# Optimization experiments

Measured on AMD Instinct MI355X. Metric: run time of the kernel, lower is better.

## Reference

```python
import jax, jax.numpy as jnp
import numpy as np

C_M, C_Z, C_H = 256, 128, 32
EPS = 1e-3      # outer-product-mean normalization eps
LN_EPS = 1e-5   # LayerNorm eps (torch default)


def setup_inputs() -> dict:
    key = jax.random.key(0)
    ks = jax.random.split(key, 8)
    B, S, R = 1, 128, 256
    m = jax.random.normal(ks[0], (B, S, R, C_M), dtype=jnp.float32)
    mask = jnp.ones((B, S, R), dtype=jnp.float32)
    ln_g = jnp.ones((C_M,), dtype=jnp.float32)
    ln_b = jnp.zeros((C_M,), dtype=jnp.float32)
    w1 = jax.random.normal(ks[1], (C_M, C_H), dtype=jnp.float32) * (1.0 / np.sqrt(C_M))
    b1 = jnp.zeros((C_H,), dtype=jnp.float32)
    w2 = jax.random.normal(ks[2], (C_M, C_H), dtype=jnp.float32) * (1.0 / np.sqrt(C_M))
    b2 = jnp.zeros((C_H,), dtype=jnp.float32)
    # linear_out uses init='final' (zeros) in training; use small random for a nontrivial baseline
    w_out = jax.random.normal(ks[3], (C_H * C_H, C_Z), dtype=jnp.float32) * 0.02
    b_out = jnp.zeros((C_Z,), dtype=jnp.float32)
    return {"m": m, "mask": mask, "ln_g": ln_g, "ln_b": ln_b,
            "w1": w1, "b1": b1, "w2": w2, "b2": b2,
            "w_out": w_out, "b_out": b_out}


def reference(m, mask, ln_g, ln_b, w1, b1, w2, b2, w_out, b_out):
    # LayerNorm over c_m
    mu = jnp.mean(m, axis=-1, keepdims=True)
    var = jnp.mean(jnp.square(m - mu), axis=-1, keepdims=True)
    mn = (m - mu) * jax.lax.rsqrt(var + LN_EPS) * ln_g + ln_b

    msk = mask[..., None]                       # [B,S,R,1]
    a = (mn @ w1 + b1) * msk                    # [B,S,R,h]
    b = (mn @ w2 + b2) * msk                    # [B,S,R,h]
    a = jnp.swapaxes(a, -2, -3)                 # [B,R,S,h]
    b = jnp.swapaxes(b, -2, -3)                 # [B,R,S,h]

    # outer product mean over the MSA (seq) dim: [B,R,R,h,h]
    outer = jnp.einsum('...isc,...jse->...ijce', a, b)
    outer = outer.reshape(*outer.shape[:-2], C_H * C_H)  # [B,R,R,h*h]
    outer = outer @ w_out + b_out               # [B,R,R,c_z]

    # normalization: pairwise count of valid MSA rows
    norm = jnp.einsum('...sia,...sja->...ija', msk, msk)  # [B,R,R,1]
    return outer / (EPS + norm)
```

## Files before the change

### kernel.cpp

```cpp
#include <hip/hip_runtime.h>

#define R   256
#define S   128
#define CM  256
#define CH  32
#define CZ  128

typedef __attribute__((ext_vector_type(8))) short short8;
typedef __attribute__((ext_vector_type(4))) float f32x4;
typedef unsigned short ushort_t;

__device__ inline ushort_t f2bf(float f) {
    union { float f; unsigned u; } v; v.f = f;
    unsigned u = v.u;
    unsigned r = u + 0x7FFF + ((u >> 16) & 1);
    return (ushort_t)(r >> 16);
}

__global__ __launch_bounds__(256) void k_prep(
    const float* __restrict__ mask, const float* __restrict__ w_out,
    const float* __restrict__ w1, const float* __restrict__ w2,
    float* __restrict__ scale, ushort_t* __restrict__ WTp,
    ushort_t* __restrict__ WcatT) {
    int b = blockIdx.x, t = threadIdx.x;
    if (b < 256) {
        int i = b, j = t;
        float acc = 0.f;
        for (int s = 0; s < S; ++s) acc += mask[s * R + i] * mask[s * R + j];
        scale[i * R + j] = 1.0f / (1e-3f + acc);
    } else if (b < 384) {
        int z = b - 256;
        #pragma unroll
        for (int q = 0; q < 4; ++q) {
            int k2 = q * 256 + t;
            int e = k2 >> 5, c = k2 & 31;
            WTp[(size_t)z * 1024 + k2] = f2bf(w_out[(size_t)(c * 32 + e) * CZ + z]);
        }
    } else {
        int ch = b - 384, k = t;
        const float* w = (ch < CH) ? w1 : w2;
        WcatT[(size_t)ch * CM + k] = f2bf(w[(size_t)k * CH + (ch & 31)]);
    }
}

__global__ __launch_bounds__(256) void k_lnproj(
    const float* __restrict__ m, const float* __restrict__ mask,
    const float* __restrict__ g, const float* __restrict__ beta,
    const float* __restrict__ b1, const float* __restrict__ b2,
    const ushort_t* __restrict__ WcatT,
    ushort_t* __restrict__ Abig, ushort_t* __restrict__ BbigT) {
    __shared__ ushort_t mnL[64 * CM];
    __shared__ ushort_t wL[64 * CM];
    int t = threadIdx.x;
    int sg = blockIdx.x & 7, rg = blockIdx.x >> 3;
    int s0 = sg * 16, r0 = rg * 4;

    int ml = t >> 2, part = t & 3;
    int r_l = ml >> 4, s_l = ml & 15;
    size_t p = (size_t)(s0 + s_l) * R + (r0 + r_l);
    const float4* row = (const float4*)(m + p * CM + part * 64);
    float4 x[16];
    float sum = 0.f, sq = 0.f;
    #pragma unroll
    for (int i = 0; i < 16; ++i) {
        x[i] = row[i];
        sum += x[i].x + x[i].y + x[i].z + x[i].w;
        sq  += x[i].x * x[i].x + x[i].y * x[i].y
             + x[i].z * x[i].z + x[i].w * x[i].w;
    }
    sum += __shfl_xor(sum, 1); sum += __shfl_xor(sum, 2);
    sq  += __shfl_xor(sq, 1);  sq  += __shfl_xor(sq, 2);
    float mean = sum * (1.0f / CM);
    float var  = sq * (1.0f / CM) - mean * mean;
    float inv  = rsqrtf(var + 1e-5f);
    const float4* g4 = (const float4*)(g + part * 64);
    const float4* be4 = (const float4*)(beta + part * 64);
    #pragma unroll
    for (int c8 = 0; c8 < 8; ++c8) {
        float4 a = x[2 * c8], b = x[2 * c8 + 1];
        float4 ga = g4[2 * c8], gb = g4[2 * c8 + 1];
        float4 ba = be4[2 * c8], bb = be4[2 * c8 + 1];
        union { ushort_t u[8]; uint4 v; } pk;
        pk.u[0] = f2bf((a.x - mean) * inv * ga.x + ba.x);
        pk.u[1] = f2bf((a.y - mean) * inv * ga.y + ba.y);
        pk.u[2] = f2bf((a.z - mean) * inv * ga.z + ba.z);
        pk.u[3] = f2bf((a.w - mean) * inv * ga.w + ba.w);
        pk.u[4] = f2bf((b.x - mean) * inv * gb.x + bb.x);
        pk.u[5] = f2bf((b.y - mean) * inv * gb.y + bb.y);
        pk.u[6] = f2bf((b.z - mean) * inv * gb.z + bb.z);
        pk.u[7] = f2bf((b.w - mean) * inv * gb.w + bb.w);
        int ck = part * 8 + c8;
        int phys = ck ^ (ml & 15);
        *(uint4*)&mnL[ml * CM + phys * 8] = pk.v;
    }
    #pragma unroll
    for (int it = 0; it < 8; ++it) {
        int v = t + it * 256;
        int ch = v >> 5, ck = v & 31;
        int phys = ck ^ (ch & 15);
        *(uint4*)&wL[ch * CM + phys * 8] =
            *(const uint4*)&WcatT[(size_t)ch * CM + ck * 8];
    }
    __syncthreads();

    int w = t >> 6, lane = t & 63, quad = lane >> 4, l15 = lane & 15;
    int ch = w * 16 + l15;
    f32x4 acc[4];
    #pragma unroll
    for (int a = 0; a < 4; a++) acc[a] = (f32x4)(0.f);
    #pragma unroll
    for (int ks = 0; ks < 8; ++ks) {
        int cb = ks * 4 + quad;
        short8 bfr = *(const short8*)&wL[ch * CM + ((cb ^ l15) << 3)];
        #pragma unroll
        for (int mt = 0; mt < 4; ++mt) {
            int mm = mt * 16 + l15;
            short8 afr = *(const short8*)&mnL[mm * CM + ((cb ^ l15) << 3)];
            acc[mt] = __builtin_amdgcn_mfma_f32_16x16x32_bf16(afr, bfr, acc[mt], 0, 0, 0);
        }
    }

    int c = ch & 31;
    float bias = (ch < CH) ? b1[c] : b2[c];
    ushort_t* dst = (ch < CH) ? Abig : BbigT;
    #pragma unroll
    for (int mt = 0; mt < 4; ++mt) {
        int r = r0 + mt;
        union { ushort_t u[4]; uint2 v; } pk;
        #pragma unroll
        for (int reg = 0; reg < 4; ++reg) {
            int s = s0 + quad * 4 + reg;
            float mv = mask[(size_t)s * R + r];
            pk.u[reg] = f2bf((acc[mt][reg] + bias) * mv);
        }
        *(uint2*)&dst[((size_t)r * CH + c) * S + s0 + quad * 4] = pk.v;
    }
}

__global__ __launch_bounds__(512, 4) void k_fuse(
    const ushort_t* __restrict__ Abig, const ushort_t* __restrict__ BbigT,
    const ushort_t* __restrict__ WTp, const float* __restrict__ b_out,
    const float* __restrict__ scale, float* __restrict__ out) {
    __shared__ ushort_t oc[64 * 128];
    __shared__ ushort_t shB[2][32 * 128];
    int t = threadIdx.x;
    int w = t >> 6, lane = t & 63, quad = lane >> 4, l15 = lane & 15;
    int ib = blockIdx.x >> 5, jb = blockIdx.x & 31;
    int i_g = ib * 8 + w;
    int jj = l15 & 7, elb = l15 >> 3;

    short8 af[2][4];
    #pragma unroll
    for (int mt = 0; mt < 2; ++mt)
        #pragma unroll
        for (int ks = 0; ks < 4; ++ks)
            af[mt][ks] = *(const short8*)
                &Abig[((size_t)i_g * 32 + mt * 16 + l15) * S + ks * 32 + quad * 8];

    int r2 = t >> 4, ck = t & 15;
    const ushort_t* gB = BbigT
        + ((size_t)jb * 256 + (r2 & 7) * 32 + (r2 >> 3)) * S + ck * 8;
    ushort_t* bdst[2];
    bdst[0] = &shB[0][r2 * 128 + ((ck ^ (r2 & 15)) << 3)];
    bdst[1] = &shB[1][r2 * 128 + ((ck ^ (r2 & 15)) << 3)];
    uint4 breg = *(const uint4*)&gB[0];

    const ushort_t* Wp = WTp + (size_t)(w * 16 + l15) * 1024 + quad * 8;
    int pwr = w * 8 + jj;

    f32x4 acc2[4];
    #pragma unroll
    for (int pt = 0; pt < 4; ++pt) acc2[pt] = (f32x4)(0.f);

    for (int ec = 0; ec < 8; ++ec) {
        int buf = ec & 1;
        *(uint4*)bdst[buf] = breg;
        if (ec < 7) breg = *(const uint4*)&gB[(ec + 1) * 512];
        __syncthreads();

        f32x4 acc1[2][2];
        #pragma unroll
        for (int a = 0; a < 2; a++)
            #pragma unroll
            for (int b = 0; b < 2; b++) acc1[a][b] = (f32x4)(0.f);
        #pragma unroll
        for (int ks = 0; ks < 4; ++ks) {
            int chq = ks * 4 + quad;
            int r20 = elb * 8 + jj;
            int r21 = r20 + 16;
            short8 bf0 = *(const short8*)
                &shB[buf][r20 * 128 + ((chq ^ (r20 & 15)) << 3)];
            short8 bf1 = *(const short8*)
                &shB[buf][r21 * 128 + ((chq ^ (r21 & 15)) << 3)];
            #pragma unroll
            for (int mt = 0; mt < 2; ++mt) {
                acc1[mt][0] = __builtin_amdgcn_mfma_f32_16x16x32_bf16(
                    af[mt][ks], bf0, acc1[mt][0], 0, 0, 0);
                acc1[mt][1] = __builtin_amdgcn_mfma_f32_16x16x32_bf16(
                    af[mt][ks], bf1, acc1[mt][1], 0, 0, 0);
            }
        }
        #pragma unroll
        for (int mt = 0; mt < 2; ++mt) {
            int c00 = mt * 16 + quad * 4;
            #pragma unroll
            for (int nt = 0; nt < 2; ++nt) {
                int el = nt * 2 + elb;
                int k2l = el * 32 + c00;
                int cc = k2l >> 3;
                union { ushort_t u[4]; uint2 v; } pk;
                #pragma unroll
                for (int reg = 0; reg < 4; ++reg)
                    pk.u[reg] = f2bf(acc1[mt][nt][reg]);
                *(uint2*)((char*)oc + pwr * 256 + ((cc ^ (pwr & 7)) << 4)
                          + ((k2l & 7) << 1)) = pk.v;
            }
        }
        __syncthreads();
        #pragma unroll
        for (int ksl = 0; ksl < 4; ++ksl) {
            short8 wf = *(const short8*)&Wp[ec * 128 + ksl * 32];
            #pragma unroll
            for (int pt = 0; pt < 4; ++pt) {
                int pp = pt * 16 + l15;
                int cc = ksl * 4 + quad;
                short8 of = *(const short8*)
                    ((const char*)oc + pp * 256 + ((cc ^ (pp & 7)) << 4));
                acc2[pt] = __builtin_amdgcn_mfma_f32_16x16x32_bf16(
                    of, wf, acc2[pt], 0, 0, 0);
            }
        }
    }

    float bz = b_out[w * 16 + l15];
    #pragma unroll
    for (int pt = 0; pt < 4; ++pt) {
        #pragma unroll
        for (int reg = 0; reg < 4; ++reg) {
            int pp = pt * 16 + quad * 4 + reg;
            int pg = (ib * 8 + (pp >> 3)) * R + jb * 8 + (pp & 7);
            out[(size_t)pg * CZ + w * 16 + l15] = (acc2[pt][reg] + bz) * scale[pg];
        }
    }
}

extern "C" void kernel_launch(void* const* d_in, const int* in_sizes, int n_in,
                              void* d_out, int out_size, void* d_ws, size_t ws_size,
                              hipStream_t stream) {
    const float* m    = (const float*)d_in[0];
    const float* mask = (const float*)d_in[1];
    const float* g    = (const float*)d_in[2];
    const float* be   = (const float*)d_in[3];
    const float* w1   = (const float*)d_in[4];
    const float* b1   = (const float*)d_in[5];
    const float* w2   = (const float*)d_in[6];
    const float* b2   = (const float*)d_in[7];
    const float* wo   = (const float*)d_in[8];
    const float* bo   = (const float*)d_in[9];
    float* out = (float*)d_out;

    char* ws = (char*)d_ws;
    ushort_t* Abig  = (ushort_t*)ws;
    ushort_t* BbigT = Abig + (size_t)R * CH * S;
    ushort_t* WTp   = BbigT + (size_t)R * CH * S;
    ushort_t* WcatT = WTp + (size_t)CZ * CH * CH;
    float*    scale = (float*)(WcatT + (size_t)64 * CM);

    k_prep<<<448, 256, 0, stream>>>(mask, wo, w1, w2, scale, WTp, WcatT);
    k_lnproj<<<512, 256, 0, stream>>>(m, mask, g, be, b1, b2, WcatT, Abig, BbigT);
    k_fuse<<<1024, 512, 0, stream>>>(Abig, BbigT, WTp, bo, scale, out);
}
```

Measured before the change: 164.4 us.

## Halve fused-kernel block size and give each wave larger register tiles

The fused outer-product/projection kernel now runs 4 waves per block instead of 8. Each wave computes two i-rows in the first GEMM and a 32x64 output tile in the second, so each B fragment and each W fragment feeds more MFMAs. The shared-memory B buffer drops from double to single buffering, which saves LDS but exposes the global loads more. Higher register use per wave may reduce occupancy, and the single buffer relies on two barriers per iteration to avoid overwrite races.

```diff
diff --git a/kernel.cpp b/kernel.cpp
--- a/kernel.cpp
+++ b/kernel.cpp
@@ -137,63 +137,68 @@
     }
 }
 
-__global__ __launch_bounds__(512, 4) void k_fuse(
+__global__ __launch_bounds__(256) void k_fuse(
     const ushort_t* __restrict__ Abig, const ushort_t* __restrict__ BbigT,
     const ushort_t* __restrict__ WTp, const float* __restrict__ b_out,
     const float* __restrict__ scale, float* __restrict__ out) {
     __shared__ ushort_t oc[64 * 128];
-    __shared__ ushort_t shB[2][32 * 128];
+    __shared__ ushort_t shB[32 * 128];
     int t = threadIdx.x;
     int w = t >> 6, lane = t & 63, quad = lane >> 4, l15 = lane & 15;
     int ib = blockIdx.x >> 5, jb = blockIdx.x & 31;
-    int i_g = ib * 8 + w;
-    int jj = l15 & 7, elb = l15 >> 3;
-
-    short8 af[2][4];
-    #pragma unroll
-    for (int mt = 0; mt < 2; ++mt)
+
+    short8 af[4][4];
+    int ibase = (ib * 8 + w * 2) * 32;
+    #pragma unroll
+    for (int mt = 0; mt < 4; ++mt)
         #pragma unroll
         for (int ks = 0; ks < 4; ++ks)
             af[mt][ks] = *(const short8*)
-                &Abig[((size_t)i_g * 32 + mt * 16 + l15) * S + ks * 32 + quad * 8];
-
-    int r2 = t >> 4, ck = t & 15;
-    const ushort_t* gB = BbigT
-        + ((size_t)jb * 256 + (r2 & 7) * 32 + (r2 >> 3)) * S + ck * 8;
-    ushort_t* bdst[2];
-    bdst[0] = &shB[0][r2 * 128 + ((ck ^ (r2 & 15)) << 3)];
-    bdst[1] = &shB[1][r2 * 128 + ((ck ^ (r2 & 15)) << 3)];
-    uint4 breg = *(const uint4*)&gB[0];
-
-    const ushort_t* Wp = WTp + (size_t)(w * 16 + l15) * 1024 + quad * 8;
-    int pwr = w * 8 + jj;
-
-    f32x4 acc2[4];
-    #pragma unroll
-    for (int pt = 0; pt < 4; ++pt) acc2[pt] = (f32x4)(0.f);
+                &Abig[(size_t)(ibase + mt * 16 + l15) * S + ks * 32 + quad * 8];
+
+    int r2a = t >> 4, cka = t & 15;
+    const ushort_t* gB0 = BbigT
+        + ((size_t)jb * 256 + (r2a & 7) * 32 + (r2a >> 3)) * S + cka * 8;
+    const ushort_t* gB1 = BbigT
+        + ((size_t)jb * 256 + (r2a & 7) * 32 + (r2a >> 3) + 2) * S + cka * 8;
+    ushort_t* bd0 = &shB[r2a * 128 + ((cka ^ (r2a & 15)) << 3)];
+    ushort_t* bd1 = &shB[(r2a + 16) * 128 + ((cka ^ ((r2a + 16) & 15)) << 3)];
+    uint4 breg0 = *(const uint4*)&gB0[0];
+    uint4 breg1 = *(const uint4*)&gB1[0];
+
+    int pg = w >> 1, zg = w & 1;
+    const ushort_t* Wp = WTp + (size_t)(zg * 64 + l15) * 1024 + quad * 8;
+
+    f32x4 acc2[2][4];
+    #pragma unroll
+    for (int a = 0; a < 2; a++)
+        #pragma unroll
+        for (int b = 0; b < 4; b++) acc2[a][b] = (f32x4)(0.f);
 
     for (int ec = 0; ec < 8; ++ec) {
-        int buf = ec & 1;
-        *(uint4*)bdst[buf] = breg;
-        if (ec < 7) breg = *(const uint4*)&gB[(ec + 1) * 512];
+        *(uint4*)bd0 = breg0;
+        *(uint4*)bd1 = breg1;
+        if (ec < 7) {
+            breg0 = *(const uint4*)&gB0[(ec + 1) * 512];
+            breg1 = *(const uint4*)&gB1[(ec + 1) * 512];
+        }
         __syncthreads();
 
-        f32x4 acc1[2][2];
-        #pragma unroll
-        for (int a = 0; a < 2; a++)
+        f32x4 acc1[4][2];
+        #pragma unroll
+        for (int a = 0; a < 4; a++)
             #pragma unroll
             for (int b = 0; b < 2; b++) acc1[a][b] = (f32x4)(0.f);
         #pragma unroll
         for (int ks = 0; ks < 4; ++ks) {
             int chq = ks * 4 + quad;
-            int r20 = elb * 8 + jj;
-            int r21 = r20 + 16;
+            int r20 = l15, r21 = 16 + l15;
             short8 bf0 = *(const short8*)
-                &shB[buf][r20 * 128 + ((chq ^ (r20 & 15)) << 3)];
+                &shB[r20 * 128 + ((chq ^ (r20 & 15)) << 3)];
             short8 bf1 = *(const short8*)
-                &shB[buf][r21 * 128 + ((chq ^ (r21 & 15)) << 3)];
-            #pragma unroll
-            for (int mt = 0; mt < 2; ++mt) {
+                &shB[r21 * 128 + ((chq ^ (r21 & 15)) << 3)];
+            #pragma unroll
+            for (int mt = 0; mt < 4; ++mt) {
                 acc1[mt][0] = __builtin_amdgcn_mfma_f32_16x16x32_bf16(
                     af[mt][ks], bf0, acc1[mt][0], 0, 0, 0);
                 acc1[mt][1] = __builtin_amdgcn_mfma_f32_16x16x32_bf16(
@@ -201,45 +206,61 @@
             }
         }
         #pragma unroll
-        for (int mt = 0; mt < 2; ++mt) {
-            int c00 = mt * 16 + quad * 4;
+        for (int mt = 0; mt < 4; ++mt) {
+            int i_l = w * 2 + (mt >> 1);
+            int pp = i_l * 8 + (l15 & 7);
+            int c0 = (mt & 1) * 16 + quad * 4;
             #pragma unroll
             for (int nt = 0; nt < 2; ++nt) {
-                int el = nt * 2 + elb;
-                int k2l = el * 32 + c00;
+                int el = nt * 2 + (l15 >> 3);
+                int k2l = el * 32 + c0;
                 int cc = k2l >> 3;
                 union { ushort_t u[4]; uint2 v; } pk;
                 #pragma unroll
                 for (int reg = 0; reg < 4; ++reg)
                     pk.u[reg] = f2bf(acc1[mt][nt][reg]);
-                *(uint2*)((char*)oc + pwr * 256 + ((cc ^ (pwr & 7)) << 4)
-                          + ((k2l & 7) << 1)) = pk.v;
+                *(uint2*)((char*)oc + pp * 256 + ((cc ^ (pp & 7)) << 4)
+                          + ((quad & 1) << 3)) = pk.v;
             }
         }
         __syncthreads();
         #pragma unroll
         for (int ksl = 0; ksl < 4; ++ksl) {
-            short8 wf = *(const short8*)&Wp[ec * 128 + ksl * 32];
-            #pragma unroll
-            for (int pt = 0; pt < 4; ++pt) {
-                int pp = pt * 16 + l15;
-                int cc = ksl * 4 + quad;
-                short8 of = *(const short8*)
-                    ((const char*)oc + pp * 256 + ((cc ^ (pp & 7)) << 4));
-                acc2[pt] = __builtin_amdgcn_mfma_f32_16x16x32_bf16(
-                    of, wf, acc2[pt], 0, 0, 0);
-            }
-        }
-    }
-
-    float bz = b_out[w * 16 + l15];
-    #pragma unroll
-    for (int pt = 0; pt < 4; ++pt) {
+            int cc2 = ksl * 4 + quad;
+            short8 a2[2];
+            #pragma unroll
+            for (int pt = 0; pt < 2; ++pt) {
+                int pp = pg * 32 + pt * 16 + l15;
+                a2[pt] = *(const short8*)
+                    ((const char*)oc + pp * 256 + ((cc2 ^ (pp & 7)) << 4));
+            }
+            #pragma unroll
+            for (int nt = 0; nt < 4; ++nt) {
+                short8 wf = *(const short8*)
+                    &Wp[(size_t)nt * 16 * 1024 + ec * 128 + ksl * 32];
+                #pragma unroll
+                for (int pt = 0; pt < 2; ++pt)
+                    acc2[pt][nt] = __builtin_amdgcn_mfma_f32_16x16x32_bf16(
+                        a2[pt], wf, acc2[pt][nt], 0, 0, 0);
+            }
+        }
+    }
+
+    float bz[4];
+    #pragma unroll
+    for (int nt = 0; nt < 4; ++nt) bz[nt] = b_out[zg * 64 + nt * 16 + l15];
+    #pragma unroll
+    for (int pt = 0; pt < 2; ++pt) {
         #pragma unroll
         for (int reg = 0; reg < 4; ++reg) {
-            int pp = pt * 16 + quad * 4 + reg;
-            int pg = (ib * 8 + (pp >> 3)) * R + jb * 8 + (pp & 7);
-            out[(size_t)pg * CZ + w * 16 + l15] = (acc2[pt][reg] + bz) * scale[pg];
+            int p = pg * 32 + pt * 16 + quad * 4 + reg;
+            int pg_glob = (ib * 8 + (p >> 3)) * R + jb * 8 + (p & 7);
+            float sc = scale[pg_glob];
+            #pragma unroll
+            for (int nt = 0; nt < 4; ++nt) {
+                int z = zg * 64 + nt * 16 + l15;
+                out[(size_t)pg_glob * CZ + z] = (acc2[pt][nt][reg] + bz[nt]) * sc;
+            }
         }
     }
 }
@@ -268,5 +289,5 @@
 
     k_prep<<<448, 256, 0, stream>>>(mask, wo, w1, w2, scale, WTp, WcatT);
     k_lnproj<<<512, 256, 0, stream>>>(m, mask, g, be, b1, b2, WcatT, Abig, BbigT);
-    k_fuse<<<1024, 512, 0, stream>>>(Abig, BbigT, WTp, bo, scale, out);
-}
+    k_fuse<<<1024, 256, 0, stream>>>(Abig, BbigT, WTp, bo, scale, out);
+}
```

Result: slower. 196.6 us (+19.6%).

## Double-buffer outer-product tile and overlap projection with next chunk

Applied to the files above, without the earlier changes.

Double-buffers the shared outer-product tile so the output-projection MFMAs for chunk ec-1 run in the same phase as the outer-product MFMAs for chunk ec. This cuts the main loop to one barrier per iteration instead of two. The projection is re-tiled so each wave computes a 32x32 block (2x2 MFMA tiles) instead of 64x16, which reduces shared-memory and weight-fragment loads per MFMA. The min-blocks launch hint is removed and shared memory per block grows, so register pressure and occupancy may change.

```diff
diff --git a/kernel.cpp b/kernel.cpp
--- a/kernel.cpp
+++ b/kernel.cpp
@@ -137,11 +137,11 @@
     }
 }
 
-__global__ __launch_bounds__(512, 4) void k_fuse(
+__global__ __launch_bounds__(512) void k_fuse(
     const ushort_t* __restrict__ Abig, const ushort_t* __restrict__ BbigT,
     const ushort_t* __restrict__ WTp, const float* __restrict__ b_out,
     const float* __restrict__ scale, float* __restrict__ out) {
-    __shared__ ushort_t oc[64 * 128];
+    __shared__ ushort_t oc[2][64 * 128];
     __shared__ ushort_t shB[2][32 * 128];
     int t = threadIdx.x;
     int w = t >> 6, lane = t & 63, quad = lane >> 4, l15 = lane & 15;
@@ -160,24 +160,49 @@
     int r2 = t >> 4, ck = t & 15;
     const ushort_t* gB = BbigT
         + ((size_t)jb * 256 + (r2 & 7) * 32 + (r2 >> 3)) * S + ck * 8;
-    ushort_t* bdst[2];
-    bdst[0] = &shB[0][r2 * 128 + ((ck ^ (r2 & 15)) << 3)];
-    bdst[1] = &shB[1][r2 * 128 + ((ck ^ (r2 & 15)) << 3)];
+    int boff = r2 * 128 + ((ck ^ (r2 & 15)) << 3);
+
+    int pg2 = w >> 2, zq = w & 3;
+    const ushort_t* Wp = WTp + (size_t)(zq * 32 + l15) * 1024 + quad * 8;
+    int pwr = w * 8 + jj;
+
+    f32x4 acc2[2][2];
+    #pragma unroll
+    for (int a = 0; a < 2; a++)
+        #pragma unroll
+        for (int b = 0; b < 2; b++) acc2[a][b] = (f32x4)(0.f);
+
+    auto stage2 = [&](int ee) {
+        const ushort_t* ob = oc[ee & 1];
+        #pragma unroll
+        for (int ksl = 0; ksl < 4; ++ksl) {
+            int cc2 = ksl * 4 + quad;
+            short8 a2[2];
+            #pragma unroll
+            for (int mt = 0; mt < 2; ++mt) {
+                int pp = pg2 * 32 + mt * 16 + l15;
+                a2[mt] = *(const short8*)
+                    ((const char*)ob + pp * 256 + ((cc2 ^ (pp & 7)) << 4));
+            }
+            #pragma unroll
+            for (int nt = 0; nt < 2; ++nt) {
+                short8 wf = *(const short8*)
+                    &Wp[(size_t)(nt * 16) * 1024 + ee * 128 + ksl * 32];
+                #pragma unroll
+                for (int mt = 0; mt < 2; ++mt)
+                    acc2[mt][nt] = __builtin_amdgcn_mfma_f32_16x16x32_bf16(
+                        a2[mt], wf, acc2[mt][nt], 0, 0, 0);
+            }
+        }
+    };
+
     uint4 breg = *(const uint4*)&gB[0];
-
-    const ushort_t* Wp = WTp + (size_t)(w * 16 + l15) * 1024 + quad * 8;
-    int pwr = w * 8 + jj;
-
-    f32x4 acc2[4];
-    #pragma unroll
-    for (int pt = 0; pt < 4; ++pt) acc2[pt] = (f32x4)(0.f);
+    *(uint4*)&shB[0][boff] = breg;
+    breg = *(const uint4*)&gB[512];
+    __syncthreads();
 
     for (int ec = 0; ec < 8; ++ec) {
         int buf = ec & 1;
-        *(uint4*)bdst[buf] = breg;
-        if (ec < 7) breg = *(const uint4*)&gB[(ec + 1) * 512];
-        __syncthreads();
-
         f32x4 acc1[2][2];
         #pragma unroll
         for (int a = 0; a < 2; a++)
@@ -186,8 +211,7 @@
         #pragma unroll
         for (int ks = 0; ks < 4; ++ks) {
             int chq = ks * 4 + quad;
-            int r20 = elb * 8 + jj;
-            int r21 = r20 + 16;
+            int r20 = l15, r21 = 16 + l15;
             short8 bf0 = *(const short8*)
                 &shB[buf][r20 * 128 + ((chq ^ (r20 & 15)) << 3)];
             short8 bf1 = *(const short8*)
@@ -212,34 +236,34 @@
                 #pragma unroll
                 for (int reg = 0; reg < 4; ++reg)
                     pk.u[reg] = f2bf(acc1[mt][nt][reg]);
-                *(uint2*)((char*)oc + pwr * 256 + ((cc ^ (pwr & 7)) << 4)
+                *(uint2*)((char*)oc[buf] + pwr * 256 + ((cc ^ (pwr & 7)) << 4)
                           + ((k2l & 7) << 1)) = pk.v;
             }
         }
+        if (ec > 0) stage2(ec - 1);
+        if (ec < 7) {
+            *(uint4*)&shB[(ec + 1) & 1][boff] = breg;
+            if (ec < 6) breg = *(const uint4*)&gB[(ec + 2) * 512];
+        }
         __syncthreads();
-        #pragma unroll
-        for (int ksl = 0; ksl < 4; ++ksl) {
-            short8 wf = *(const short8*)&Wp[ec * 128 + ksl * 32];
-            #pragma unroll
-            for (int pt = 0; pt < 4; ++pt) {
-                int pp = pt * 16 + l15;
-                int cc = ksl * 4 + quad;
-                short8 of = *(const short8*)
-                    ((const char*)oc + pp * 256 + ((cc ^ (pp & 7)) << 4));
-                acc2[pt] = __builtin_amdgcn_mfma_f32_16x16x32_bf16(
-                    of, wf, acc2[pt], 0, 0, 0);
-            }
-        }
-    }
-
-    float bz = b_out[w * 16 + l15];
-    #pragma unroll
-    for (int pt = 0; pt < 4; ++pt) {
+    }
+    stage2(7);
+
+    float bz[2];
+    #pragma unroll
+    for (int nt = 0; nt < 2; ++nt) bz[nt] = b_out[zq * 32 + nt * 16 + l15];
+    #pragma unroll
+    for (int mt = 0; mt < 2; ++mt) {
         #pragma unroll
         for (int reg = 0; reg < 4; ++reg) {
-            int pp = pt * 16 + quad * 4 + reg;
-            int pg = (ib * 8 + (pp >> 3)) * R + jb * 8 + (pp & 7);
-            out[(size_t)pg * CZ + w * 16 + l15] = (acc2[pt][reg] + bz) * scale[pg];
+            int p = pg2 * 32 + mt * 16 + quad * 4 + reg;
+            int pg_glob = (ib * 8 + (p >> 3)) * R + jb * 8 + (p & 7);
+            float sc = scale[pg_glob];
+            #pragma unroll
+            for (int nt = 0; nt < 2; ++nt) {
+                int z = zq * 32 + nt * 16 + l15;
+                out[(size_t)pg_glob * CZ + z] = (acc2[mt][nt][reg] + bz[nt]) * sc;
+            }
         }
     }
 }
```

New measurement: 185.9 us. +13.1%, slower.
